# Kernel tuning notes

Hardware: AMD Instinct MI355X
Metric: run time of the kernel (lower is better)

The kernel has to match this reference:

```python
import jax, jax.numpy as jnp
import numpy as np
import math

HEAD_DIM = 64
NQ = 24          # num query heads
NKV = 4          # num kv heads
HIDDEN = 1536
WINDOW = 256     # sliding window (layer_idx=0 -> active)
THETA = 10000.0
EPS = 1e-6


def _rope(x, cos, sin):
    # x: [B,S,H,D]; cos/sin: [S,1,D//2]  (broadcast over B and heads)
    xr = x.reshape(*x.shape[:-1], -1, 2)
    x1, x2 = xr[..., 0], xr[..., 1]
    r = jnp.stack([x1 * cos - x2 * sin, x2 * cos + x1 * sin], axis=-1)
    return r.reshape(x.shape)


def setup_inputs() -> dict:
    key = jax.random.key(0)
    k1, k2, k3 = jax.random.split(key, 3)
    B, S = 2, 2048
    x = jax.random.normal(k1, (B, S, HIDDEN), dtype=jnp.float32)
    norm_scale = jnp.ones((HIDDEN,), dtype=jnp.float32)             # RMSNorm scale
    w_qkv = jax.random.normal(k2, ((NQ + 2 * NKV) * HEAD_DIM, HIDDEN), dtype=jnp.float32) * 0.02
    w_out = jax.random.normal(k3, (HIDDEN, NQ * HEAD_DIM), dtype=jnp.float32) * 0.02
    return {"x": x, "norm_scale": norm_scale, "w_qkv": w_qkv, "w_out": w_out, "start_pos": 0}


def reference(x, norm_scale, w_qkv, w_out, start_pos):
    B, S, _ = x.shape
    # RMSNorm
    var = jnp.mean(x * x, axis=-1, keepdims=True)
    xn = x * jax.lax.rsqrt(var + EPS) * norm_scale
    # QKV projection (nn.Linear: x @ W^T)
    qkv = xn @ w_qkv.T
    qs, kvs = NQ * HEAD_DIM, NKV * HEAD_DIM
    q = qkv[..., :qs].reshape(B, S, NQ, HEAD_DIM)
    k = qkv[..., qs:qs + kvs].reshape(B, S, NKV, HEAD_DIM)
    v = qkv[..., qs + kvs:].reshape(B, S, NKV, HEAD_DIM)
    # RoPE
    inv_freq = 1.0 / (THETA ** (jnp.arange(0, HEAD_DIM, 2, dtype=jnp.float32) / HEAD_DIM))
    t = jnp.arange(start_pos, start_pos + S, dtype=jnp.float32)
    freqs = t[:, None] * inv_freq[None, :]                       # [S, D//2]
    cos, sin = jnp.cos(freqs)[:, None, :], jnp.sin(freqs)[:, None, :]
    q = _rope(q, cos, sin)
    k = _rope(k, cos, sin)
    # GQA: expand kv heads (repeat_interleave over head dim)
    rep = NQ // NKV
    k = jnp.repeat(k, rep, axis=2)
    v = jnp.repeat(v, rep, axis=2)
    # attention with causal + sliding-window mask
    scale = 1.0 / math.sqrt(HEAD_DIM)
    scores = jnp.einsum('bqhd,bkhd->bhqk', q * scale, k)        # [B,H,S,S]
    ipos = start_pos + jnp.arange(S)
    j = jnp.arange(S)
    mask = (j[None, :] > ipos[:, None]) | (j[None, :] < ipos[:, None] - WINDOW)
    scores = jnp.where(mask[None, None], -jnp.inf, scores)
    probs = jax.nn.softmax(scores, axis=-1)
    attn = jnp.einsum('bhqk,bkhd->bqhd', probs, v).reshape(B, S, NQ * HEAD_DIM)
    # output projection + residual
    return x + attn @ w_out.T
```

## Files before the change

### kernel.cpp

```cpp
#include <hip/hip_runtime.h>
#include <hip/hip_bf16.h>

typedef float f32x4 __attribute__((ext_vector_type(4)));
typedef short s16x8 __attribute__((ext_vector_type(8)));
typedef unsigned short u16;

#define B_ 2
#define S_ 2048
#define HID 1536
#define NQ_ 24
#define NKV_ 4
#define HD 64
#define NTOK (B_*S_)
#define QKVN ((NQ_+2*NKV_)*HD)

#define CVT_BLKS  ((QKVN*HID + HID*HID)/4/256)
#define RMS_BLKS  NTOK
#define TAB_BLKS  (S_*32/256)
#define SETUP_BLKS (CVT_BLKS + RMS_BLKS + TAB_BLKS)

#define ROPE2_BLOCKS ((NTOK*28*16)/256)
#define VT_BLOCKS (B_*NKV_*(S_/64))

#define LDS_FENCE() asm volatile("" ::: "memory")

#define WAITBAR(n) asm volatile("s_waitcnt vmcnt(" #n ")\n\ts_barrier" ::: "memory")
#define RAWBAR()   asm volatile("s_barrier" ::: "memory")

__device__ __forceinline__ float bf2f(u16 u) {
  unsigned int x = ((unsigned int)u) << 16;
  float f; __builtin_memcpy(&f, &x, 4); return f;
}
__device__ __forceinline__ u16 f2bf(float f) {
  unsigned int u; __builtin_memcpy(&u, &f, 4);
  u += 0x7fffu + ((u >> 16) & 1u);
  return (u16)(u >> 16);
}
__device__ __forceinline__ unsigned long long pk4bf(float a, float b, float c, float d) {
  __hip_bfloat162 x = __float22bfloat162_rn(make_float2(a, b));
  __hip_bfloat162 y = __float22bfloat162_rn(make_float2(c, d));
  unsigned int xi, yi;
  __builtin_memcpy(&xi, &x, 4);
  __builtin_memcpy(&yi, &y, 4);
  return (unsigned long long)xi | ((unsigned long long)yi << 32);
}

__global__ __launch_bounds__(256) void k_setup(const float* __restrict__ x,
                                               const float* __restrict__ g,
                                               const float* __restrict__ wq,
                                               const float* __restrict__ wo,
                                               u16* __restrict__ wb,
                                               u16* __restrict__ xn,
                                               float2* __restrict__ tab,
                                               const int* __restrict__ spp) {
  int bid = blockIdx.x, tid = threadIdx.x;
  if (bid < CVT_BLKS) {
    int i = bid * 256 + tid;
    const int n0q = QKVN*HID/4;
    const float* src = (i < n0q) ? wq : wo;
    int j = (i < n0q) ? i : i - n0q;
    f32x4 v = ((const f32x4*)src)[j];
    *(unsigned long long*)(wb + (size_t)i*4) = pk4bf(v[0], v[1], v[2], v[3]);
  } else if (bid < CVT_BLKS + RMS_BLKS) {
    int row = bid - CVT_BLKS;
    const f32x4* xr = (const f32x4*)(x + (size_t)row * HID);
    f32x4 v0 = {}, v1 = {};
    float ss = 0.f;
    if (tid < 192) {
      v0 = xr[2*tid]; v1 = xr[2*tid + 1];
      ss = v0[0]*v0[0] + v0[1]*v0[1] + v0[2]*v0[2] + v0[3]*v0[3]
         + v1[0]*v1[0] + v1[1]*v1[1] + v1[2]*v1[2] + v1[3]*v1[3];
    }
#pragma unroll
    for (int off = 1; off < 64; off <<= 1) ss += __shfl_xor(ss, off);
    __shared__ float red[4];
    if ((tid & 63) == 0) red[tid >> 6] = ss;
    __syncthreads();
    float rs = rsqrtf((red[0] + red[1] + red[2] + red[3]) * (1.f/HID) + 1e-6f);
    if (tid < 192) {
      const f32x4* gr = (const f32x4*)g;
      f32x4 g0 = gr[2*tid], g1 = gr[2*tid + 1];
      unsigned long long* out = (unsigned long long*)(xn + (size_t)row * HID);
      out[2*tid]     = pk4bf(v0[0]*rs*g0[0], v0[1]*rs*g0[1], v0[2]*rs*g0[2], v0[3]*rs*g0[3]);
      out[2*tid + 1] = pk4bf(v1[0]*rs*g1[0], v1[1]*rs*g1[1], v1[2]*rs*g1[2], v1[3]*rs*g1[3]);
    }
  } else {
    int i = (bid - CVT_BLKS - RMS_BLKS) * 256 + tid;
    int s = i >> 5, p = i & 31;
    float t = (float)(spp[0] + s);
    float inv = exp2f((float)p * -0.41524101186f);
    float sn, cs;
    sincosf(t * inv, &sn, &cs);
    tab[i] = make_float2(cs, sn);
  }
}

template <bool F32OUT>
__global__ __launch_bounds__(256) void k_gemm_bt(const u16* __restrict__ A,
                                                 const u16* __restrict__ W,
                                                 void* __restrict__ Cv,
                                                 const float* __restrict__ resid,
                                                 int N, int K) {
  __shared__ __align__(16) u16 As0[128*64], Bs0[64*64];
  __shared__ __align__(16) u16 As1[128*64], Bs1[64*64];
  int lin = blockIdx.x;
  int xcd = lin & 7, loc = lin >> 3;
  int mloc = loc & 3, nloc = loc >> 2;
  int m0 = (xcd*4 + mloc) * 128, n0 = nloc * 64;
  int tid = threadIdx.x;
  int w = tid >> 6, l = tid & 63;
  int wr = w >> 1, wc = w & 1;
  int c = l & 15, g = l >> 4;
  f32x4 acc[4][2] = {};
  int r8 = l >> 3;
  int sslot = (l & 7) ^ r8;
  const u16* Ag = A + (size_t)(m0 + w*32 + r8)*K + sslot*8;
  const u16* Wg = W + (size_t)(n0 + w*16 + r8)*K + sslot*8;

#define STAGE(dA, dB, k0) do {                                                          \
  _Pragma("unroll")                                                                     \
  for (int i = 0; i < 4; i++)                                                           \
    __builtin_amdgcn_global_load_lds(                                                   \
        (const __attribute__((address_space(1))) void*)(Ag + (size_t)(i*8)*K + (k0)),   \
        (__attribute__((address_space(3))) void*)(dA + (w*32 + i*8)*64), 16, 0, 0);     \
  _Pragma("unroll")                                                                     \
  for (int i = 0; i < 2; i++)                                                           \
    __builtin_amdgcn_global_load_lds(                                                   \
        (const __attribute__((address_space(1))) void*)(Wg + (size_t)(i*8)*K + (k0)),   \
        (__attribute__((address_space(3))) void*)(dB + (w*16 + i*8)*64), 16, 0, 0);     \
  } while (0)

#define COMPUTE(sA, sB) do {                                                            \
  _Pragma("unroll")                                                                     \
  for (int ks = 0; ks < 2; ks++) {                                                      \
    s16x8 af[4], bq[2];                                                                 \
    int sl = ((ks*4 + g) ^ (c & 7)) * 8;                                                \
    _Pragma("unroll")                                                                   \
    for (int mt = 0; mt < 4; mt++)                                                      \
      af[mt] = *(const s16x8*)(sA + (wr*64 + mt*16 + c)*64 + sl);                       \
    _Pragma("unroll")                                                                   \
    for (int nt = 0; nt < 2; nt++)                                                      \
      bq[nt] = *(const s16x8*)(sB + (wc*32 + nt*16 + c)*64 + sl);                       \
    _Pragma("unroll")                                                                   \
    for (int mt = 0; mt < 4; mt++)                                                      \
      _Pragma("unroll")                                                                 \
      for (int nt = 0; nt < 2; nt++)                                                    \
        acc[mt][nt] = __builtin_amdgcn_mfma_f32_16x16x32_bf16(af[mt], bq[nt],           \
                                                              acc[mt][nt], 0, 0, 0);    \
  } } while (0)

  const int NT = K >> 6;
  STAGE(As0, Bs0, 0);
  STAGE(As1, Bs1, 64);
  WAITBAR(6);
  for (int t = 0; t + 2 < NT; t += 2) {
    COMPUTE(As0, Bs0);
    RAWBAR();
    STAGE(As0, Bs0, (t+2)*64);
    WAITBAR(6);
    COMPUTE(As1, Bs1);
    RAWBAR();
    if (t + 3 < NT) {
      STAGE(As1, Bs1, (t+3)*64);
      WAITBAR(6);
    } else {
      WAITBAR(0);
    }
  }
  COMPUTE(As0, Bs0);
  WAITBAR(0);
  COMPUTE(As1, Bs1);
#undef STAGE
#undef COMPUTE

#pragma unroll
  for (int mt = 0; mt < 4; mt++)
#pragma unroll
    for (int nt = 0; nt < 2; nt++)
#pragma unroll
      for (int r = 0; r < 4; r++) {
        int m = m0 + wr*64 + mt*16 + g*4 + r;
        int n = n0 + wc*32 + nt*16 + c;
        size_t off = (size_t)m*N + n;
        float vv = acc[mt][nt][r];
        if (F32OUT) {
          ((float*)Cv)[off] = vv + resid[off];
        } else {
          ((u16*)Cv)[off] = f2bf(vv);
        }
      }
}

__global__ __launch_bounds__(256) void k_rope_vt(const u16* __restrict__ qkv,
                                                 u16* __restrict__ q,
                                                 u16* __restrict__ k,
                                                 u16* __restrict__ vt,
                                                 const float2* __restrict__ tab) {
  __shared__ u16 tile[64][65];
  int bid = blockIdx.x;
  if (bid < ROPE2_BLOCKS) {
    int idx = bid * 256 + threadIdx.x;
    int j = idx & 15;
    int h = (idx >> 4) % 28;
    int tok = idx / 448;
    int s = tok & (S_ - 1);
    int b = tok >> 11;
    f32x4 cs = *(const f32x4*)(tab + (size_t)s*32 + 2*j);
    int col = (h < NQ_) ? h*64 + 4*j : HID + (h - NQ_)*64 + 4*j;
    unsigned long long pr = *(const unsigned long long*)(qkv + (size_t)tok*QKVN + col);
    float x1a = bf2f((u16)pr),         x2a = bf2f((u16)(pr >> 16));
    float x1b = bf2f((u16)(pr >> 32)), x2b = bf2f((u16)(pr >> 48));
    float ya1 = x1a*cs[0] - x2a*cs[1];
    float ya2 = x2a*cs[0] + x1a*cs[1];
    float yb1 = x1b*cs[2] - x2b*cs[3];
    float yb2 = x2b*cs[2] + x1b*cs[3];
    unsigned long long outp = pk4bf(ya1, ya2, yb1, yb2);
    if (h < NQ_) {
      *(unsigned long long*)(q + (((size_t)(b*NQ_ + h))*S_ + s)*64 + 4*j) = outp;
    } else {
      *(unsigned long long*)(k + (((size_t)(b*NKV_ + (h - NQ_)))*S_ + s)*64 + 4*j) = outp;
    }
  } else {
    int blk = bid - ROPE2_BLOCKS;
    int st = blk & 31;
    int hk = (blk >> 5) & 3;
    int b = blk >> 7;
    int s0 = st * 64;
#pragma unroll
    for (int i = 0; i < 16; i++) {
      int ii = threadIdx.x + i*256;
      int r = ii >> 6, cc = ii & 63;
      tile[r][cc] = qkv[((size_t)(b*S_) + s0 + r)*QKVN + (NQ_+NKV_)*64 + hk*64 + cc];
    }
    __syncthreads();
#pragma unroll
    for (int i = 0; i < 16; i++) {
      int ii = threadIdx.x + i*256;
      int d = ii >> 6, s = ii & 63;
      vt[((size_t)(b*NKV_ + hk)*64 + d)*S_ + s0 + s] = tile[s][d];
    }
  }
}

__global__ __launch_bounds__(64, 3) void k_attn(const u16* __restrict__ q,
                                                const u16* __restrict__ k,
                                                const u16* __restrict__ vt,
                                                u16* __restrict__ ao,
                                                const int* __restrict__ spp) {
  __shared__ __align__(16) u16 Pt[32*72];
  int lin = blockIdx.x;
  int xcd = lin & 7, loc = lin >> 3;
  int qb = loc & 63;
  int bh = xcd * 6 + (loc >> 6);
  int h = bh % NQ_;
  int b = bh / NQ_;
  int q0 = qb * 32;
  int hk = h / (NQ_/NKV_);
  int l = threadIdx.x;
  int c = l & 15, g = l >> 4;
  int sp = spp[0];
  const u16* qptr = q + ((size_t)(b*NQ_ + h))*S_*64;
  const u16* kptr = k + ((size_t)(b*NKV_ + hk))*S_*64;
  const u16* vptr = vt + ((size_t)(b*NKV_ + hk))*64*S_;

  s16x8 qf[2][2];
#pragma unroll
  for (int qt = 0; qt < 2; qt++)
#pragma unroll
    for (int ks = 0; ks < 2; ks++)
      qf[qt][ks] = *(const s16x8*)(qptr + (size_t)(q0 + qt*16 + c)*64 + ks*32 + g*8);

  f32x4 o[4][2] = {};
  float m_run[2], l_run[2];
#pragma unroll
  for (int i = 0; i < 2; i++) { m_run[i] = -1e30f; l_run[i] = 0.f; }

  int lo = sp + q0 - 256; if (lo < 0) lo = 0;
  int hi = sp + q0 + 31;  if (hi > S_ - 1) hi = S_ - 1;
  int kt0 = lo >> 6, kt1 = hi >> 6;

  s16x8 kf[4][2];
#pragma unroll
  for (int km = 0; km < 4; km++)
#pragma unroll
    for (int ks = 0; ks < 2; ks++)
      kf[km][ks] = *(const s16x8*)(kptr + (size_t)(kt0*64 + km*16 + c)*64 + ks*32 + g*8);

  for (int kt = kt0; kt <= kt1; kt++) {
    s16x8 vf[2][4];
#pragma unroll
    for (int ks = 0; ks < 2; ks++)
#pragma unroll
      for (int dt = 0; dt < 4; dt++)
        vf[ks][dt] = *(const s16x8*)(vptr + (size_t)(dt*16 + c)*S_ + kt*64 + ks*32 + g*8);

    bool full = (kt*64 + 63 <= sp + q0) && (kt*64 >= sp + q0 - 225);
#pragma unroll
    for (int qt = 0; qt < 2; qt++) {
      f32x4 sa[4];
      __builtin_amdgcn_s_setprio(1);
#pragma unroll
      for (int km = 0; km < 4; km++) {
        f32x4 z = {};
        z = __builtin_amdgcn_mfma_f32_16x16x32_bf16(kf[km][0], qf[qt][0], z, 0, 0, 0);
        sa[km] = __builtin_amdgcn_mfma_f32_16x16x32_bf16(kf[km][1], qf[qt][1], z, 0, 0, 0);
      }
      __builtin_amdgcn_s_setprio(0);
      if (qt == 1 && kt < kt1) {
#pragma unroll
        for (int km = 0; km < 4; km++)
#pragma unroll
          for (int ks = 0; ks < 2; ks++)
            kf[km][ks] = *(const s16x8*)(kptr + (size_t)((kt+1)*64 + km*16 + c)*64 + ks*32 + g*8);
      }
      float mx = -1e30f;
      if (full) {
#pragma unroll
        for (int km = 0; km < 4; km++)
#pragma unroll
          for (int r = 0; r < 4; r++) {
            float sv = sa[km][r] * 0.125f;
            sa[km][r] = sv;
            mx = fmaxf(mx, sv);
          }
      } else {
        int pos = sp + q0 + qt*16 + c;
#pragma unroll
        for (int km = 0; km < 4; km++)
#pragma unroll
          for (int r = 0; r < 4; r++) {
            int key = kt*64 + km*16 + g*4 + r;
            float sv = sa[km][r] * 0.125f;
            sv = ((unsigned)(pos - key) <= 256u) ? sv : -1e30f;
            sa[km][r] = sv;
            mx = fmaxf(mx, sv);
          }
      }
      mx = fmaxf(mx, __shfl_xor(mx, 16));
      mx = fmaxf(mx, __shfl_xor(mx, 32));
      float mnew = fmaxf(m_run[qt], mx);
      float alpha = __expf(m_run[qt] - mnew);
      m_run[qt] = mnew;
      float rsum = 0.f;
#pragma unroll
      for (int km = 0; km < 4; km++) {
        float p0 = __expf(sa[km][0] - mnew);
        float p1 = __expf(sa[km][1] - mnew);
        float p2 = __expf(sa[km][2] - mnew);
        float p3 = __expf(sa[km][3] - mnew);
        rsum += p0 + p1 + p2 + p3;
        *(unsigned long long*)(Pt + (qt*16 + c)*72 + km*16 + g*4) = pk4bf(p0, p1, p2, p3);
      }
      rsum += __shfl_xor(rsum, 16);
      rsum += __shfl_xor(rsum, 32);
      l_run[qt] = l_run[qt]*alpha + rsum;
#pragma unroll
      for (int dt = 0; dt < 4; dt++) {
        o[dt][qt][0] *= alpha; o[dt][qt][1] *= alpha;
        o[dt][qt][2] *= alpha; o[dt][qt][3] *= alpha;
      }
    }
    LDS_FENCE();
    __builtin_amdgcn_s_setprio(1);
#pragma unroll
    for (int ks = 0; ks < 2; ks++)
#pragma unroll
      for (int qt = 0; qt < 2; qt++) {
        s16x8 pf = *(const s16x8*)(Pt + (qt*16 + c)*72 + ks*32 + g*8);
#pragma unroll
        for (int dt = 0; dt < 4; dt++)
          o[dt][qt] = __builtin_amdgcn_mfma_f32_16x16x32_bf16(vf[ks][dt], pf, o[dt][qt], 0, 0, 0);
      }
    __builtin_amdgcn_s_setprio(0);
    LDS_FENCE();
  }
#pragma unroll
  for (int qt = 0; qt < 2; qt++) {
    float inv = 1.f / l_run[qt];
    int qi = q0 + qt*16 + c;
    u16* row = ao + ((size_t)(b*S_) + qi)*HID + h*64;
#pragma unroll
    for (int dt = 0; dt < 4; dt++)
      *(unsigned long long*)(row + dt*16 + g*4) =
          pk4bf(o[dt][qt][0]*inv, o[dt][qt][1]*inv, o[dt][qt][2]*inv, o[dt][qt][3]*inv);
  }
}

extern "C" void kernel_launch(void* const* d_in, const int* in_sizes, int n_in,
                              void* d_out, int out_size, void* d_ws, size_t ws_size,
                              hipStream_t stream) {
  const float* x_f32    = (const float*)d_in[0];
  const float* g_f32    = (const float*)d_in[1];
  const float* wqkv_f32 = (const float*)d_in[2];
  const float* wout_f32 = (const float*)d_in[3];
  const int*   spp      = (const int*)d_in[4];
  char* ws = (char*)d_ws;
  u16* wqkvb = (u16*)(ws);
  u16* woutb = (u16*)(ws + 6291456);
  u16* xn    = (u16*)(ws + 11010048);
  u16* qkv   = (u16*)(ws + 23592960);
  u16* qbuf  = (u16*)(ws + 40370176);
  u16* kbuf  = (u16*)(ws + 52953088);
  u16* vtb   = (u16*)(ws + 55050240);
  u16* attn  = xn;
  float2* tab = (float2*)d_out;

  k_setup<<<SETUP_BLKS, 256, 0, stream>>>(x_f32, g_f32, wqkv_f32, wout_f32,
                                          wqkvb, xn, tab, spp);
  k_gemm_bt<false><<<32*(QKVN/64), 256, 0, stream>>>(xn, wqkvb, qkv, nullptr, QKVN, HID);
  k_rope_vt<<<ROPE2_BLOCKS + VT_BLOCKS, 256, 0, stream>>>(qkv, qbuf, kbuf, vtb,
                                                          (const float2*)tab);
  k_attn<<<B_*NQ_*(S_/32), 64, 0, stream>>>(qbuf, kbuf, vtb, attn, spp);
  k_gemm_bt<true><<<32*(HID/64), 256, 0, stream>>>(attn, woutb, d_out, x_f32, HID, HID);
}
```

Baseline: 202.9 us.

## Halve GEMM K-tile with occupancy hint and skip lazy softmax rescaling

The projection GEMM now stages 32-wide K slices instead of 64 into smaller shared buffers and requests four blocks per CU. The point is to raise occupancy and hide load latency better, at the cost of twice as many barrier and stage iterations. Separately, the attention softmax only rescales the running max, sum and output accumulators when a new row max exceeds the stored one by more than a threshold. This skips most per-tile alpha multiplications but allows exponentials up to e^8 in the bf16 probabilities.

```diff
diff --git a/kernel.cpp b/kernel.cpp
--- a/kernel.cpp
+++ b/kernel.cpp
@@ -96,13 +96,13 @@
 }
 
 template <bool F32OUT>
-__global__ __launch_bounds__(256) void k_gemm_bt(const u16* __restrict__ A,
-                                                 const u16* __restrict__ W,
-                                                 void* __restrict__ Cv,
-                                                 const float* __restrict__ resid,
-                                                 int N, int K) {
-  __shared__ __align__(16) u16 As0[128*64], Bs0[64*64];
-  __shared__ __align__(16) u16 As1[128*64], Bs1[64*64];
+__global__ __launch_bounds__(256, 4) void k_gemm_bt(const u16* __restrict__ A,
+                                                    const u16* __restrict__ W,
+                                                    void* __restrict__ Cv,
+                                                    const float* __restrict__ resid,
+                                                    int N, int K) {
+  __shared__ __align__(16) u16 As0[128*32], Bs0[64*32];
+  __shared__ __align__(16) u16 As1[128*32], Bs1[64*32];
   int lin = blockIdx.x;
   int xcd = lin & 7, loc = lin >> 3;
   int mloc = loc & 3, nloc = loc >> 2;
@@ -112,57 +112,53 @@
   int wr = w >> 1, wc = w & 1;
   int c = l & 15, g = l >> 4;
   f32x4 acc[4][2] = {};
-  int r8 = l >> 3;
-  int sslot = (l & 7) ^ r8;
-  const u16* Ag = A + (size_t)(m0 + w*32 + r8)*K + sslot*8;
-  const u16* Wg = W + (size_t)(n0 + w*16 + r8)*K + sslot*8;
+  int r16 = l >> 2;
+  int sslot = (l & 3) ^ (r16 & 3);
+  const u16* Ag = A + (size_t)(m0 + w*32 + r16)*K + sslot*8;
+  const u16* Wg = W + (size_t)(n0 + w*16 + r16)*K + sslot*8;
 
 #define STAGE(dA, dB, k0) do {                                                          \
-  _Pragma("unroll")                                                                     \
-  for (int i = 0; i < 4; i++)                                                           \
-    __builtin_amdgcn_global_load_lds(                                                   \
-        (const __attribute__((address_space(1))) void*)(Ag + (size_t)(i*8)*K + (k0)),   \
-        (__attribute__((address_space(3))) void*)(dA + (w*32 + i*8)*64), 16, 0, 0);     \
   _Pragma("unroll")                                                                     \
   for (int i = 0; i < 2; i++)                                                           \
     __builtin_amdgcn_global_load_lds(                                                   \
-        (const __attribute__((address_space(1))) void*)(Wg + (size_t)(i*8)*K + (k0)),   \
-        (__attribute__((address_space(3))) void*)(dB + (w*16 + i*8)*64), 16, 0, 0);     \
+        (const __attribute__((address_space(1))) void*)(Ag + (size_t)(i*16)*K + (k0)),  \
+        (__attribute__((address_space(3))) void*)(dA + (w*32 + i*16)*32), 16, 0, 0);    \
+  __builtin_amdgcn_global_load_lds(                                                     \
+      (const __attribute__((address_space(1))) void*)(Wg + (k0)),                       \
+      (__attribute__((address_space(3))) void*)(dB + (w*16)*32), 16, 0, 0);             \
   } while (0)
 
 #define COMPUTE(sA, sB) do {                                                            \
-  _Pragma("unroll")                                                                     \
-  for (int ks = 0; ks < 2; ks++) {                                                      \
     s16x8 af[4], bq[2];                                                                 \
-    int sl = ((ks*4 + g) ^ (c & 7)) * 8;                                                \
+    int sl = (g ^ (c & 3)) * 8;                                                         \
     _Pragma("unroll")                                                                   \
     for (int mt = 0; mt < 4; mt++)                                                      \
-      af[mt] = *(const s16x8*)(sA + (wr*64 + mt*16 + c)*64 + sl);                       \
+      af[mt] = *(const s16x8*)(sA + (wr*64 + mt*16 + c)*32 + sl);                       \
     _Pragma("unroll")                                                                   \
     for (int nt = 0; nt < 2; nt++)                                                      \
-      bq[nt] = *(const s16x8*)(sB + (wc*32 + nt*16 + c)*64 + sl);                       \
+      bq[nt] = *(const s16x8*)(sB + (wc*32 + nt*16 + c)*32 + sl);                       \
     _Pragma("unroll")                                                                   \
     for (int mt = 0; mt < 4; mt++)                                                      \
       _Pragma("unroll")                                                                 \
       for (int nt = 0; nt < 2; nt++)                                                    \
         acc[mt][nt] = __builtin_amdgcn_mfma_f32_16x16x32_bf16(af[mt], bq[nt],           \
                                                               acc[mt][nt], 0, 0, 0);    \
-  } } while (0)
-
-  const int NT = K >> 6;
+  } while (0)
+
+  const int NT = K >> 5;
   STAGE(As0, Bs0, 0);
-  STAGE(As1, Bs1, 64);
-  WAITBAR(6);
+  STAGE(As1, Bs1, 32);
+  WAITBAR(3);
   for (int t = 0; t + 2 < NT; t += 2) {
     COMPUTE(As0, Bs0);
     RAWBAR();
-    STAGE(As0, Bs0, (t+2)*64);
-    WAITBAR(6);
+    STAGE(As0, Bs0, (t+2)*32);
+    WAITBAR(3);
     COMPUTE(As1, Bs1);
     RAWBAR();
     if (t + 3 < NT) {
-      STAGE(As1, Bs1, (t+3)*64);
-      WAITBAR(6);
+      STAGE(As1, Bs1, (t+3)*32);
+      WAITBAR(3);
     } else {
       WAITBAR(0);
     }
@@ -338,27 +334,31 @@
       }
       mx = fmaxf(mx, __shfl_xor(mx, 16));
       mx = fmaxf(mx, __shfl_xor(mx, 32));
-      float mnew = fmaxf(m_run[qt], mx);
-      float alpha = __expf(m_run[qt] - mnew);
-      m_run[qt] = mnew;
+      if (__ballot(mx > m_run[qt] + 8.f) != 0) {
+        float mnew = fmaxf(m_run[qt], mx);
+        float alpha = __expf(m_run[qt] - mnew);
+        m_run[qt] = mnew;
+        l_run[qt] *= alpha;
+#pragma unroll
+        for (int dt = 0; dt < 4; dt++) {
+          o[dt][qt][0] *= alpha; o[dt][qt][1] *= alpha;
+          o[dt][qt][2] *= alpha; o[dt][qt][3] *= alpha;
+        }
+      }
+      float mref = m_run[qt];
       float rsum = 0.f;
 #pragma unroll
       for (int km = 0; km < 4; km++) {
-        float p0 = __expf(sa[km][0] - mnew);
-        float p1 = __expf(sa[km][1] - mnew);
-        float p2 = __expf(sa[km][2] - mnew);
-        float p3 = __expf(sa[km][3] - mnew);
+        float p0 = __expf(sa[km][0] - mref);
+        float p1 = __expf(sa[km][1] - mref);
+        float p2 = __expf(sa[km][2] - mref);
+        float p3 = __expf(sa[km][3] - mref);
         rsum += p0 + p1 + p2 + p3;
         *(unsigned long long*)(Pt + (qt*16 + c)*72 + km*16 + g*4) = pk4bf(p0, p1, p2, p3);
       }
       rsum += __shfl_xor(rsum, 16);
       rsum += __shfl_xor(rsum, 32);
-      l_run[qt] = l_run[qt]*alpha + rsum;
-#pragma unroll
-      for (int dt = 0; dt < 4; dt++) {
-        o[dt][qt][0] *= alpha; o[dt][qt][1] *= alpha;
-        o[dt][qt][2] *= alpha; o[dt][qt][3] *= alpha;
-      }
+      l_run[qt] += rsum;
     }
     LDS_FENCE();
     __builtin_amdgcn_s_setprio(1);
```

After: 216.2 us. 1.07x slower.
